# Performance work log

Hardware: AMD Instinct MI355X
Metric: run time of the kernel (lower is better)

Reference implementation:

```python
import jax, jax.numpy as jnp
import numpy as np

DIM, HEADS, HEAD_DIM = 1024, 16, 64
B, L, S = 4, 2048, 2048
EPS = 1e-5
NEG_INF = -1e9


def rms_norm(x, w):
    # x: [..., d]; normalize over last dim, scale by learned weight w [d]
    var = jnp.mean(jnp.square(x), axis=-1, keepdims=True)
    return x * jax.lax.rsqrt(var + EPS) * w


def setup_inputs() -> dict:
    key = jax.random.key(0)
    ks = jax.random.split(key, 9)
    hd = HEADS * HEAD_DIM
    scale = 1.0 / np.sqrt(DIM)
    return {
        "q": jax.random.normal(ks[0], (B, L, DIM), dtype=jnp.float32),
        "kv": jax.random.normal(ks[1], (B, S, DIM), dtype=jnp.float32),
        "x_seqlens": jax.random.randint(ks[2], (B,), 1, S + 1, dtype=jnp.int32),
        "Wq": jax.random.normal(ks[3], (DIM, hd), dtype=jnp.float32) * scale,
        "Wk": jax.random.normal(ks[4], (DIM, hd), dtype=jnp.float32) * scale,
        "Wv": jax.random.normal(ks[5], (DIM, hd), dtype=jnp.float32) * scale,
        "Wo": jax.random.normal(ks[6], (hd, DIM), dtype=jnp.float32) * (1.0 / np.sqrt(hd)),
        "q_norm_w": jnp.ones((HEAD_DIM,), dtype=jnp.float32),
        "k_norm_w": jnp.ones((HEAD_DIM,), dtype=jnp.float32),
    }


def reference(q, kv, x_seqlens, Wq, Wk, Wv, Wo, q_norm_w, k_norm_w):
    b, l, _ = q.shape
    s = kv.shape[1]
    # QKV projections -> [b, h, n, d]
    qh = (q @ Wq).reshape(b, l, HEADS, HEAD_DIM).transpose(0, 2, 1, 3)
    kh = (kv @ Wk).reshape(b, s, HEADS, HEAD_DIM).transpose(0, 2, 1, 3)
    vh = (kv @ Wv).reshape(b, s, HEADS, HEAD_DIM).transpose(0, 2, 1, 3)
    # per-head RMSNorm on q and k
    qh = rms_norm(qh, q_norm_w)
    kh = rms_norm(kh, k_norm_w)
    # dense padding mask [b, 1, 1, s]: True where kv position is valid
    mask = (jnp.arange(s, dtype=jnp.int32)[None, :] < x_seqlens[:, None])[:, None, None, :]
    # scaled dot-product attention (math path: full score matrix)
    scores = jnp.einsum("bhld,bhsd->bhls", qh, kh) * (1.0 / np.sqrt(HEAD_DIM))
    scores = jnp.where(mask, scores, NEG_INF)
    attn = jax.nn.softmax(scores, axis=-1)
    o = jnp.einsum("bhls,bhsd->bhld", attn, vh)  # [b, h, l, d]
    o = o.transpose(0, 2, 1, 3).reshape(b, l, HEADS * HEAD_DIM)
    return o @ Wo
```

## Files before the change

kernel.cpp:

```cpp
#include <hip/hip_runtime.h>
#include <hip/hip_bf16.h>
#include <stdint.h>

#define BB 4
#define LL 2048
#define SS 2048
#define DIMM 1024
#define HH 16
#define HD 64
#define NHD 1024

typedef __bf16 bf16_t;
typedef __bf16 bf16x8 __attribute__((ext_vector_type(8)));
typedef __bf16 bf16x4 __attribute__((ext_vector_type(4)));
typedef float f32x4 __attribute__((ext_vector_type(4)));

#define GLDS16(g, l) __builtin_amdgcn_global_load_lds( \
    (const __attribute__((address_space(1))) void*)(g), \
    (__attribute__((address_space(3))) void*)(l), 16, 0, 0)

#define FENCED_BARRIER() do {                    \
    asm volatile("" ::: "memory");               \
    __builtin_amdgcn_s_barrier();                \
    asm volatile("" ::: "memory");               \
    __builtin_amdgcn_sched_barrier(0);           \
  } while (0)

#define SWZ(o) ((o) ^ ((((o) >> 7) & 7) << 4))

__global__ __launch_bounds__(256) void cvt_all(const float* __restrict__ q,
                                               const float* __restrict__ kv,
                                               bf16_t* __restrict__ Aq,
                                               bf16_t* __restrict__ Akv) {
  const int bi = blockIdx.x;
  const float* in = (bi < 4096) ? q : kv;
  bf16_t* out = (bi < 4096) ? Aq : Akv;
  size_t i = ((size_t)(bi & 4095) * 256 + threadIdx.x) * 8;
  const f32x4* p = (const f32x4*)(in + i);
  f32x4 a = p[0], b = p[1];
  bf16x8 o;
#pragma unroll
  for (int j = 0; j < 4; ++j) { o[j] = (bf16_t)a[j]; o[4 + j] = (bf16_t)b[j]; }
  *(bf16x8*)(out + i) = o;
}

__global__ __launch_bounds__(256) void transpose_all(
    const float* __restrict__ W0, const float* __restrict__ W1,
    const float* __restrict__ W2, const float* __restrict__ W3,
    bf16_t* __restrict__ O0, bf16_t* __restrict__ O1,
    bf16_t* __restrict__ O2, bf16_t* __restrict__ O3) {
  const float* in = (blockIdx.z == 0) ? W0 : (blockIdx.z == 1) ? W1
                    : (blockIdx.z == 2) ? W2 : W3;
  bf16_t* out = (blockIdx.z == 0) ? O0 : (blockIdx.z == 1) ? O1
                : (blockIdx.z == 2) ? O2 : O3;
  __shared__ float tile[64][65];
  const int r0 = blockIdx.y * 64, c0 = blockIdx.x * 64;
  const int tr = threadIdx.x >> 2;
  const int tc4 = (threadIdx.x & 3) * 16;
#pragma unroll
  for (int i = 0; i < 4; ++i) {
    f32x4 v = *(const f32x4*)&in[(size_t)(r0 + tr) * 1024 + c0 + tc4 + i * 4];
    tile[tr][tc4 + i * 4 + 0] = v.x;
    tile[tr][tc4 + i * 4 + 1] = v.y;
    tile[tr][tc4 + i * 4 + 2] = v.z;
    tile[tr][tc4 + i * 4 + 3] = v.w;
  }
  __syncthreads();
#pragma unroll
  for (int i = 0; i < 2; ++i) {
    bf16x8 o;
#pragma unroll
    for (int j = 0; j < 8; ++j) o[j] = (bf16_t)tile[tc4 + i * 8 + j][tr];
    *(bf16x8*)&out[(size_t)(c0 + tr) * 1024 + r0 + tc4 + i * 8] = o;
  }
}

__global__ __launch_bounds__(512, 1) void proj_qkv(
    const bf16_t* __restrict__ Aq, const bf16_t* __restrict__ Akv,
    const bf16_t* __restrict__ WqT, const bf16_t* __restrict__ WkT,
    const bf16_t* __restrict__ WvT,
    bf16_t* __restrict__ Qb, bf16_t* __restrict__ Kb, bf16_t* __restrict__ Vt,
    const float* __restrict__ qw, const float* __restrict__ kw, float qscale) {
  __shared__ bf16_t Lds[2][4][8192];
  const int nt = blockIdx.x;
  const int mode = nt >> 2;
  const bf16_t* A  = (mode == 0) ? Aq : Akv;
  const bf16_t* Bt = (mode == 0) ? WqT : (mode == 1 ? WkT : WvT);
  const int n0 = (nt & 3) * 256;
  const int m0 = blockIdx.y * 256;
  const int tid = threadIdx.x, lane = tid & 63, w = tid >> 6;
  const int wr = w >> 2, wc = w & 3;
  const int fr = lane & 15, fg = lane >> 4;
  f32x4 acc[8][4] = {};

  auto stageKT = [&](int kt, int d) {
#pragma unroll
    for (int ht = 0; ht < 4; ++ht) {
#pragma unroll
      for (int c = 0; c < 2; ++c) {
        const int o = (c * 512 + tid) * 16;
        const int eff = SWZ(o);
        const int rl = eff >> 7, ce = (eff & 127) >> 1;
        const bf16_t* src = (ht < 2)
            ? A  + (size_t)(m0 + ht * 128 + rl) * 1024 + kt * 64 + ce
            : Bt + (size_t)(n0 + (ht - 2) * 128 + rl) * 1024 + kt * 64 + ce;
        GLDS16(src, &Lds[d][ht][c * 4096 + w * 512]);
      }
    }
  };

  stageKT(0, 0);
  int cur = 0;
  for (int kt = 0; kt < 16; ++kt) {
    if (kt + 1 < 16) {
      stageKT(kt + 1, cur ^ 1);
      asm volatile("s_waitcnt vmcnt(8)" ::: "memory");
    } else {
      asm volatile("s_waitcnt vmcnt(0)" ::: "memory");
    }
    FENCED_BARRIER();

    bf16x8 bfr[4][2];
#pragma unroll
    for (int n = 0; n < 4; ++n)
#pragma unroll
      for (int ks = 0; ks < 2; ++ks) {
        const int o = ((wc & 1) * 64 + n * 16 + fr) * 128 + ks * 64 + fg * 16;
        bfr[n][ks] = *(const bf16x8*)&Lds[cur][2 + (wc >> 1)][SWZ(o) >> 1];
      }
    bf16x8 af[2][4];
#pragma unroll
    for (int ks = 0; ks < 2; ++ks)
#pragma unroll
      for (int m2 = 0; m2 < 2; ++m2) {
        const int o = (m2 * 16 + fr) * 128 + ks * 64 + fg * 16;
        af[0][m2 * 2 + ks] = *(const bf16x8*)&Lds[cur][wr][SWZ(o) >> 1];
      }

#pragma unroll
    for (int q = 0; q < 4; ++q) {
      asm volatile("s_waitcnt lgkmcnt(0)" ::: "memory");
      __builtin_amdgcn_sched_barrier(0);
      if (q < 3) {
#pragma unroll
        for (int ks = 0; ks < 2; ++ks)
#pragma unroll
          for (int m2 = 0; m2 < 2; ++m2) {
            const int o = ((q + 1) * 32 + m2 * 16 + fr) * 128 + ks * 64 + fg * 16;
            af[(q + 1) & 1][m2 * 2 + ks] =
                *(const bf16x8*)&Lds[cur][wr][SWZ(o) >> 1];
          }
      }
      __builtin_amdgcn_s_setprio(1);
#pragma unroll
      for (int m2 = 0; m2 < 2; ++m2)
#pragma unroll
        for (int n = 0; n < 4; ++n)
#pragma unroll
          for (int ks = 0; ks < 2; ++ks)
            acc[q * 2 + m2][n] = __builtin_amdgcn_mfma_f32_16x16x32_bf16(
                af[q & 1][m2 * 2 + ks], bfr[n][ks], acc[q * 2 + m2][n], 0, 0, 0);
      __builtin_amdgcn_s_setprio(0);
      FENCED_BARRIER();
    }
    cur ^= 1;
  }

  if (mode <= 1) {
    const float* nw = (mode == 0) ? qw : kw;
    const float ps = (mode == 0) ? qscale : 1.0f;
    bf16_t* Cb = (mode == 0) ? Qb : Kb;
    float w4[4];
#pragma unroll
    for (int n = 0; n < 4; ++n) w4[n] = nw[n * 16 + fr] * ps;
#pragma unroll
    for (int m = 0; m < 8; ++m) {
      float ss[4];
#pragma unroll
      for (int j = 0; j < 4; ++j) {
        ss[j] = 0.f;
#pragma unroll
        for (int n = 0; n < 4; ++n) ss[j] += acc[m][n][j] * acc[m][n][j];
      }
#pragma unroll
      for (int d = 1; d < 16; d <<= 1)
#pragma unroll
        for (int j = 0; j < 4; ++j) ss[j] += __shfl_xor(ss[j], d);
      float rs[4];
#pragma unroll
      for (int j = 0; j < 4; ++j) rs[j] = rsqrtf(ss[j] * (1.f / 64.f) + 1e-5f);
#pragma unroll
      for (int n = 0; n < 4; ++n)
#pragma unroll
        for (int j = 0; j < 4; ++j) {
          size_t row = (size_t)m0 + wr * 128 + m * 16 + fg * 4 + j;
          size_t col = (size_t)n0 + wc * 64 + n * 16 + fr;
          Cb[row * NHD + col] = (bf16_t)(acc[m][n][j] * rs[j] * w4[n]);
        }
    }
  } else {
#pragma unroll
    for (int m = 0; m < 8; ++m) {
      int r = m0 + wr * 128 + m * 16 + fg * 4;
      int bb_ = r >> 11, s0 = r & 2047;
#pragma unroll
      for (int n = 0; n < 4; ++n) {
        int cc = n0 + wc * 64 + n * 16 + fr;
        int hh_ = cc >> 6, dd = cc & 63;
        bf16x4 pk;
#pragma unroll
        for (int j = 0; j < 4; ++j) pk[j] = (bf16_t)acc[m][n][j];
        *(bf16x4*)&Vt[(((size_t)bb_ * 16 + hh_) * 64 + dd) * 2048 + s0] = pk;
      }
    }
  }
}

__global__ __launch_bounds__(256) void gemm_out(const bf16_t* __restrict__ A,
                                                const bf16_t* __restrict__ Bt,
                                                float* __restrict__ Cout) {
  __shared__ bf16_t As[2][4096];
  __shared__ bf16_t Bs[2][4096];
  const int K = 1024, N = 1024;
  const int tid = threadIdx.x, lane = tid & 63, w = tid >> 6;
  const int m0 = blockIdx.y * 128, n0 = blockIdx.x * 128;
  const int wm = (w >> 1) * 64, wn = (w & 1) * 64;
  const int fr = lane & 15, fg = lane >> 4;
  f32x4 acc[4][4] = {};

  auto stage = [&](int kt, int bi) {
    const int kb = kt * 32;
#pragma unroll
    for (int j = 0; j < 2; ++j) {
      int e = (j * 4 + w) * 512 + lane * 8;
      int r = e >> 5, c = e & 31;
      GLDS16(A  + (size_t)(m0 + r) * K + kb + c, &As[bi][(j * 4 + w) * 512]);
      GLDS16(Bt + (size_t)(n0 + r) * K + kb + c, &Bs[bi][(j * 4 + w) * 512]);
    }
  };

  stage(0, 0);
  int cur = 0;
  for (int kt = 0; kt < 32; ++kt) {
    if (kt + 1 < 32) {
      stage(kt + 1, cur ^ 1);
      asm volatile("s_waitcnt vmcnt(4)" ::: "memory");
    } else {
      asm volatile("s_waitcnt vmcnt(0)" ::: "memory");
    }
    FENCED_BARRIER();
    bf16x8 a[4], b[4];
#pragma unroll
    for (int m = 0; m < 4; ++m) a[m] = *(const bf16x8*)&As[cur][(wm + m * 16 + fr) * 32 + fg * 8];
#pragma unroll
    for (int n = 0; n < 4; ++n) b[n] = *(const bf16x8*)&Bs[cur][(wn + n * 16 + fr) * 32 + fg * 8];
    __builtin_amdgcn_s_setprio(1);
#pragma unroll
    for (int m = 0; m < 4; ++m)
#pragma unroll
      for (int n = 0; n < 4; ++n)
        acc[m][n] = __builtin_amdgcn_mfma_f32_16x16x32_bf16(a[m], b[n], acc[m][n], 0, 0, 0);
    __builtin_amdgcn_s_setprio(0);
    FENCED_BARRIER();
    cur ^= 1;
  }
#pragma unroll
  for (int m = 0; m < 4; ++m)
#pragma unroll
    for (int n = 0; n < 4; ++n)
#pragma unroll
      for (int j = 0; j < 4; ++j) {
        size_t row = (size_t)m0 + wm + m * 16 + fg * 4 + j;
        size_t col = (size_t)n0 + wn + n * 16 + fr;
        Cout[row * N + col] = acc[m][n][j];
      }
}

__global__ __launch_bounds__(256, 3) void attn64(const bf16_t* __restrict__ Qb,
                                                 const bf16_t* __restrict__ Kb,
                                                 const bf16_t* __restrict__ Vtg,
                                                 bf16_t* __restrict__ Ob,
                                                 const int* __restrict__ seqlens) {
  __shared__ bf16_t Kl[2][4096];
  __shared__ bf16_t Vl[2][4096];
  __shared__ bf16_t Pl[8192];
  const int tid = threadIdx.x, lane = tid & 63, w = tid >> 6;
  const int fr = lane & 15, fg = lane >> 4;
  const int qt = blockIdx.x, bh = blockIdx.y;
  const int b = bh >> 4, h = bh & 15;
  const int seqlen = seqlens[b];
  const int ntiles = (seqlen + 63) >> 6;
  bf16_t* Pw = &Pl[w * 2048];

  const bf16_t* qp = Qb + ((size_t)b * LL + qt * 128 + w * 32 + fr) * NHD + h * 64;
  bf16x8 qf[2][2];
#pragma unroll
  for (int qs = 0; qs < 2; ++qs) {
    qf[qs][0] = *(const bf16x8*)&qp[(size_t)qs * 16 * NHD + fg * 8];
    qf[qs][1] = *(const bf16x8*)&qp[(size_t)qs * 16 * NHD + 32 + fg * 8];
  }
  asm volatile("s_waitcnt vmcnt(0)" ::: "memory");

  const bf16_t* Kg = Kb + (size_t)b * SS * NHD + h * 64;
  const bf16_t* Vg = Vtg + ((size_t)(b * 16 + h)) * 64 * SS;

  auto stage = [&](int t, int bi) {
#pragma unroll
    for (int c = 0; c < 2; ++c) {
      const int ro = (w * 2 + c) * 8 + (lane >> 3);
      const int cs = ((lane & 7) ^ (ro & 7)) * 8;
      GLDS16(Kg + (size_t)(t * 64 + ro) * NHD + cs, &Kl[bi][(w * 2 + c) * 512]);
      GLDS16(Vg + (size_t)ro * SS + t * 64 + cs, &Vl[bi][(w * 2 + c) * 512]);
    }
  };

  bf16x8 vones;
#pragma unroll
  for (int i = 0; i < 8; ++i) vones[i] = (bf16_t)1.0f;

  f32x4 oacc[2][4] = {};
  f32x4 lacc[2] = {};
  const float M0 = 12.0f;

  auto softmax_strip = [&](f32x4 (&s)[4], int qs, int t) {
    if (t == ntiles - 1 && (seqlen & 63)) {
#pragma unroll
      for (int n = 0; n < 4; ++n) {
        bool valid = (t * 64 + n * 16 + fr) < seqlen;
#pragma unroll
        for (int j = 0; j < 4; ++j) s[n][j] = valid ? s[n][j] : -1e30f;
      }
    }
#pragma unroll
    for (int n = 0; n < 4; ++n)
#pragma unroll
      for (int j = 0; j < 4; ++j) s[n][j] = __builtin_exp2f(s[n][j] - M0);
#pragma unroll
    for (int n = 0; n < 4; ++n)
#pragma unroll
      for (int j = 0; j < 4; ++j) {
        const int prow = qs * 16 + fg * 4 + j;
        const int pcol = n * 16 + fr;
        Pw[prow * 64 + (((pcol >> 3) ^ (prow & 7)) * 8) + (pcol & 7)] =
            (bf16_t)s[n][j];
      }
  };

  stage(0, 0);
  int cur = 0;
  for (int t = 0; t < ntiles; ++t) {
    if (t + 1 < ntiles) {
      stage(t + 1, cur ^ 1);
      asm volatile("s_waitcnt vmcnt(4)" ::: "memory");
    } else {
      asm volatile("s_waitcnt vmcnt(0)" ::: "memory");
    }
    FENCED_BARRIER();

    f32x4 s0[4] = {}, s1[4] = {};
    __builtin_amdgcn_s_setprio(1);
#pragma unroll
    for (int n = 0; n < 4; ++n) {
      const int rr = n * 16 + fr;
      bf16x8 kf0 = *(const bf16x8*)&Kl[cur][rr * 64 + ((fg ^ (rr & 7)) * 8)];
      bf16x8 kf1 = *(const bf16x8*)&Kl[cur][rr * 64 + (((fg + 4) ^ (rr & 7)) * 8)];
      s0[n] = __builtin_amdgcn_mfma_f32_16x16x32_bf16(qf[0][0], kf0, s0[n], 0, 0, 0);
      s0[n] = __builtin_amdgcn_mfma_f32_16x16x32_bf16(qf[0][1], kf1, s0[n], 0, 0, 0);
      s1[n] = __builtin_amdgcn_mfma_f32_16x16x32_bf16(qf[1][0], kf0, s1[n], 0, 0, 0);
      s1[n] = __builtin_amdgcn_mfma_f32_16x16x32_bf16(qf[1][1], kf1, s1[n], 0, 0, 0);
    }
    __builtin_amdgcn_s_setprio(0);

    softmax_strip(s0, 0, t);
    softmax_strip(s1, 1, t);

    asm volatile("s_waitcnt lgkmcnt(0)" ::: "memory");
    __builtin_amdgcn_sched_barrier(0);

    __builtin_amdgcn_s_setprio(1);
#pragma unroll
    for (int ks = 0; ks < 2; ++ks) {
      const int pr0 = fr, pr1 = 16 + fr;
      bf16x8 pa0 = *(const bf16x8*)&Pw[pr0 * 64 + (((ks * 4 + fg) ^ (pr0 & 7)) * 8)];
      bf16x8 pa1 = *(const bf16x8*)&Pw[pr1 * 64 + (((ks * 4 + fg) ^ (pr1 & 7)) * 8)];
#pragma unroll
      for (int n = 0; n < 4; ++n) {
        const int rr = n * 16 + fr;
        bf16x8 vf = *(const bf16x8*)&Vl[cur][rr * 64 + (((ks * 4 + fg) ^ (rr & 7)) * 8)];
        oacc[0][n] = __builtin_amdgcn_mfma_f32_16x16x32_bf16(pa0, vf, oacc[0][n], 0, 0, 0);
        oacc[1][n] = __builtin_amdgcn_mfma_f32_16x16x32_bf16(pa1, vf, oacc[1][n], 0, 0, 0);
      }
      lacc[0] = __builtin_amdgcn_mfma_f32_16x16x32_bf16(pa0, vones, lacc[0], 0, 0, 0);
      lacc[1] = __builtin_amdgcn_mfma_f32_16x16x32_bf16(pa1, vones, lacc[1], 0, 0, 0);
    }
    __builtin_amdgcn_s_setprio(0);
    FENCED_BARRIER();
    cur ^= 1;
  }

#pragma unroll
  for (int qs = 0; qs < 2; ++qs) {
    float inv[4];
#pragma unroll
    for (int j = 0; j < 4; ++j) inv[j] = __builtin_amdgcn_rcpf(lacc[qs][j]);
#pragma unroll
    for (int n = 0; n < 4; ++n)
#pragma unroll
      for (int j = 0; j < 4; ++j) {
        size_t row = (size_t)b * LL + qt * 128 + w * 32 + qs * 16 + fg * 4 + j;
        Ob[row * NHD + h * 64 + n * 16 + fr] = (bf16_t)(oacc[qs][n][j] * inv[j]);
      }
  }
}

extern "C" void kernel_launch(void* const* d_in, const int* in_sizes, int n_in,
                              void* d_out, int out_size, void* d_ws, size_t ws_size,
                              hipStream_t stream) {
  const float* q   = (const float*)d_in[0];
  const float* kv  = (const float*)d_in[1];
  const int* seqlens = (const int*)d_in[2];
  const float* Wq = (const float*)d_in[3];
  const float* Wk = (const float*)d_in[4];
  const float* Wv = (const float*)d_in[5];
  const float* Wo = (const float*)d_in[6];
  const float* qw = (const float*)d_in[7];
  const float* kw = (const float*)d_in[8];

  char* ws = (char*)d_ws;
  const size_t MB = 1 << 20;
  bf16_t* Aq  = (bf16_t*)(ws + 0 * MB);
  bf16_t* Akv = (bf16_t*)(ws + 16 * MB);
  bf16_t* WqT = (bf16_t*)(ws + 32 * MB);
  bf16_t* WkT = (bf16_t*)(ws + 34 * MB);
  bf16_t* WvT = (bf16_t*)(ws + 36 * MB);
  bf16_t* WoT = (bf16_t*)(ws + 38 * MB);
  bf16_t* Qb  = (bf16_t*)(ws + 40 * MB);
  bf16_t* Kb  = (bf16_t*)(ws + 56 * MB);
  bf16_t* Vt  = (bf16_t*)(ws + 72 * MB);

  const float QSCALE = 0.125f * 1.44269504088896f;

  cvt_all<<<8192, 256, 0, stream>>>(q, kv, Aq, Akv);
  dim3 tg(16, 16, 4);
  transpose_all<<<tg, 256, 0, stream>>>(Wq, Wk, Wv, Wo, WqT, WkT, WvT, WoT);
  dim3 pg(12, 32);
  proj_qkv<<<pg, 512, 0, stream>>>(Aq, Akv, WqT, WkT, WvT, Qb, Kb, Vt,
                                   qw, kw, QSCALE);
  dim3 ag(LL / 128, BB * HH);
  attn64<<<ag, 256, 0, stream>>>(Qb, Kb, Vt, Aq, seqlens);
  dim3 og(8, 64);
  gemm_out<<<og, 256, 0, stream>>>(Aq, WoT, (float*)d_out);
}
```

Baseline: 193.4 us.

## Shrink QKV projection tile to 256x128 to double block count

The fused QKV projection kernel now uses a 256x128 output tile instead of 256x256. The grid doubles to 768 blocks, and each of the 8 waves computes a 64x64 sub-tile laid out as 4 rows by 2 columns. The intent is better CU occupancy and load balance on the many-CU GPU, since 384 blocks was a poor fit. The inner loop is also simplified: the four-phase software-pipelined A-fragment loads with per-phase barriers are replaced by loading all fragments, then running one MFMA burst. The cost is lower arithmetic intensity per block, with more global and LDS traffic per FLOP, and less overlap of LDS reads with MFMA.

```diff
diff --git a/kernel.cpp b/kernel.cpp
--- a/kernel.cpp
+++ b/kernel.cpp
@@ -81,21 +81,21 @@
     const bf16_t* __restrict__ WvT,
     bf16_t* __restrict__ Qb, bf16_t* __restrict__ Kb, bf16_t* __restrict__ Vt,
     const float* __restrict__ qw, const float* __restrict__ kw, float qscale) {
-  __shared__ bf16_t Lds[2][4][8192];
+  __shared__ bf16_t Lds[2][3][8192];
   const int nt = blockIdx.x;
-  const int mode = nt >> 2;
+  const int mode = nt >> 3;
   const bf16_t* A  = (mode == 0) ? Aq : Akv;
   const bf16_t* Bt = (mode == 0) ? WqT : (mode == 1 ? WkT : WvT);
-  const int n0 = (nt & 3) * 256;
+  const int n0 = (nt & 7) * 128;
   const int m0 = blockIdx.y * 256;
   const int tid = threadIdx.x, lane = tid & 63, w = tid >> 6;
-  const int wr = w >> 2, wc = w & 3;
+  const int wr = w >> 1, wc = w & 1;
   const int fr = lane & 15, fg = lane >> 4;
-  f32x4 acc[8][4] = {};
+  f32x4 acc[4][4] = {};
 
   auto stageKT = [&](int kt, int d) {
 #pragma unroll
-    for (int ht = 0; ht < 4; ++ht) {
+    for (int ht = 0; ht < 3; ++ht) {
 #pragma unroll
       for (int c = 0; c < 2; ++c) {
         const int o = (c * 512 + tid) * 16;
@@ -103,7 +103,7 @@
         const int rl = eff >> 7, ce = (eff & 127) >> 1;
         const bf16_t* src = (ht < 2)
             ? A  + (size_t)(m0 + ht * 128 + rl) * 1024 + kt * 64 + ce
-            : Bt + (size_t)(n0 + (ht - 2) * 128 + rl) * 1024 + kt * 64 + ce;
+            : Bt + (size_t)(n0 + rl) * 1024 + kt * 64 + ce;
         GLDS16(src, &Lds[d][ht][c * 4096 + w * 512]);
       }
     }
@@ -114,55 +114,40 @@
   for (int kt = 0; kt < 16; ++kt) {
     if (kt + 1 < 16) {
       stageKT(kt + 1, cur ^ 1);
-      asm volatile("s_waitcnt vmcnt(8)" ::: "memory");
+      asm volatile("s_waitcnt vmcnt(6)" ::: "memory");
     } else {
       asm volatile("s_waitcnt vmcnt(0)" ::: "memory");
     }
     FENCED_BARRIER();
 
-    bf16x8 bfr[4][2];
+    bf16x8 af[4][2], bf[4][2];
+#pragma unroll
+    for (int m = 0; m < 4; ++m)
+#pragma unroll
+      for (int ks = 0; ks < 2; ++ks) {
+        const int row = wr * 64 + m * 16 + fr;
+        const int o = (row & 127) * 128 + ks * 64 + fg * 16;
+        af[m][ks] = *(const bf16x8*)&Lds[cur][row >> 7][SWZ(o) >> 1];
+      }
 #pragma unroll
     for (int n = 0; n < 4; ++n)
 #pragma unroll
       for (int ks = 0; ks < 2; ++ks) {
-        const int o = ((wc & 1) * 64 + n * 16 + fr) * 128 + ks * 64 + fg * 16;
-        bfr[n][ks] = *(const bf16x8*)&Lds[cur][2 + (wc >> 1)][SWZ(o) >> 1];
-      }
-    bf16x8 af[2][4];
-#pragma unroll
-    for (int ks = 0; ks < 2; ++ks)
-#pragma unroll
-      for (int m2 = 0; m2 < 2; ++m2) {
-        const int o = (m2 * 16 + fr) * 128 + ks * 64 + fg * 16;
-        af[0][m2 * 2 + ks] = *(const bf16x8*)&Lds[cur][wr][SWZ(o) >> 1];
-      }
-
-#pragma unroll
-    for (int q = 0; q < 4; ++q) {
-      asm volatile("s_waitcnt lgkmcnt(0)" ::: "memory");
-      __builtin_amdgcn_sched_barrier(0);
-      if (q < 3) {
+        const int row = wc * 64 + n * 16 + fr;
+        const int o = row * 128 + ks * 64 + fg * 16;
+        bf[n][ks] = *(const bf16x8*)&Lds[cur][2][SWZ(o) >> 1];
+      }
+    __builtin_amdgcn_s_setprio(1);
+#pragma unroll
+    for (int m = 0; m < 4; ++m)
+#pragma unroll
+      for (int n = 0; n < 4; ++n)
 #pragma unroll
         for (int ks = 0; ks < 2; ++ks)
-#pragma unroll
-          for (int m2 = 0; m2 < 2; ++m2) {
-            const int o = ((q + 1) * 32 + m2 * 16 + fr) * 128 + ks * 64 + fg * 16;
-            af[(q + 1) & 1][m2 * 2 + ks] =
-                *(const bf16x8*)&Lds[cur][wr][SWZ(o) >> 1];
-          }
-      }
-      __builtin_amdgcn_s_setprio(1);
-#pragma unroll
-      for (int m2 = 0; m2 < 2; ++m2)
-#pragma unroll
-        for (int n = 0; n < 4; ++n)
-#pragma unroll
-          for (int ks = 0; ks < 2; ++ks)
-            acc[q * 2 + m2][n] = __builtin_amdgcn_mfma_f32_16x16x32_bf16(
-                af[q & 1][m2 * 2 + ks], bfr[n][ks], acc[q * 2 + m2][n], 0, 0, 0);
-      __builtin_amdgcn_s_setprio(0);
-      FENCED_BARRIER();
-    }
+          acc[m][n] = __builtin_amdgcn_mfma_f32_16x16x32_bf16(
+              af[m][ks], bf[n][ks], acc[m][n], 0, 0, 0);
+    __builtin_amdgcn_s_setprio(0);
+    FENCED_BARRIER();
     cur ^= 1;
   }
 
@@ -174,7 +159,7 @@
 #pragma unroll
     for (int n = 0; n < 4; ++n) w4[n] = nw[n * 16 + fr] * ps;
 #pragma unroll
-    for (int m = 0; m < 8; ++m) {
+    for (int m = 0; m < 4; ++m) {
       float ss[4];
 #pragma unroll
       for (int j = 0; j < 4; ++j) {
@@ -193,15 +178,15 @@
       for (int n = 0; n < 4; ++n)
 #pragma unroll
         for (int j = 0; j < 4; ++j) {
-          size_t row = (size_t)m0 + wr * 128 + m * 16 + fg * 4 + j;
+          size_t row = (size_t)m0 + wr * 64 + m * 16 + fg * 4 + j;
           size_t col = (size_t)n0 + wc * 64 + n * 16 + fr;
           Cb[row * NHD + col] = (bf16_t)(acc[m][n][j] * rs[j] * w4[n]);
         }
     }
   } else {
 #pragma unroll
-    for (int m = 0; m < 8; ++m) {
-      int r = m0 + wr * 128 + m * 16 + fg * 4;
+    for (int m = 0; m < 4; ++m) {
+      int r = m0 + wr * 64 + m * 16 + fg * 4;
       int bb_ = r >> 11, s0 = r & 2047;
 #pragma unroll
       for (int n = 0; n < 4; ++n) {
@@ -443,7 +428,7 @@
   cvt_all<<<8192, 256, 0, stream>>>(q, kv, Aq, Akv);
   dim3 tg(16, 16, 4);
   transpose_all<<<tg, 256, 0, stream>>>(Wq, Wk, Wv, Wo, WqT, WkT, WvT, WoT);
-  dim3 pg(12, 32);
+  dim3 pg(24, 32);
   proj_qkv<<<pg, 512, 0, stream>>>(Aq, Akv, WqT, WkT, WvT, Qb, Kb, Vt,
                                    qw, kw, QSCALE);
   dim3 ag(LL / 128, BB * HH);
```

New measurement: 187.6 us. -3.0%, faster.
